# Kernel tuning notes

Hardware: AMD Instinct MI355X
Metric: run time of the kernel (lower is better)

Reference implementation:

```python
import jax, jax.numpy as jnp
import numpy as np

B, N = 16, 16384


def square_distance(a, b):
    # a [B,S,3], b [B,N,3] -> squared pairwise distance [B,S,N]
    return (jnp.sum(a * a, -1)[:, :, None]
            + jnp.sum(b * b, -1)[:, None, :]
            - 2.0 * jnp.einsum('bsc,bnc->bsn', a, b))


def fps(xyz, npoint):
    # farthest point sampling (deterministic start at index 0).
    b, n, _ = xyz.shape

    def step(carry, _):
        dist, far = carry
        cen = jnp.take_along_axis(xyz, far[:, None, None], axis=1)  # [B,1,3]
        d = jnp.sum((xyz - cen) ** 2, -1)
        dist = jnp.minimum(dist, d)
        return (dist, jnp.argmax(dist, -1)), far

    init = (jnp.full((b, n), 1e10, xyz.dtype), jnp.zeros((b,), jnp.int32))
    _, idx = jax.lax.scan(step, init, None, length=npoint)
    return idx.T  # [B, npoint]


def query_ball(radius, nsample, xyz, new_xyz):
    # torch query_ball_point: mark out-of-radius as N, sort, take first nsample,
    # replace leftover N with the first valid index.
    b, n, _ = xyz.shape
    sqr = square_distance(new_xyz, xyz)                      # [B,S,N]
    idx = jnp.broadcast_to(jnp.arange(n), sqr.shape)
    idx = jnp.where(sqr > radius * radius, n, idx)
    idx = jnp.sort(idx, axis=-1)[:, :, :nsample]             # [B,S,K]
    first = idx[:, :, :1]
    return jnp.where(idx == n, first, idx)


def index_points(points, idx):
    # points [B,N,C], idx [B,...] -> [B,...,C]
    return jax.vmap(lambda p, i: p[i])(points, idx)


def set_abstraction(xyz, points, npoint, radius, nsample, weights):
    new_xyz = index_points(xyz, fps(xyz, npoint))            # [B,S,3]
    idx = query_ball(radius, nsample, xyz, new_xyz)          # [B,S,K]
    grouped_xyz = index_points(xyz, idx) - new_xyz[:, :, None, :]  # [B,S,K,3]
    if points is None:
        feat = grouped_xyz
    else:
        feat = jnp.concatenate([grouped_xyz, index_points(points, idx)], axis=-1)
    for W, b_ in weights:                                    # 1x1 conv == per-point linear
        feat = jax.nn.relu(jnp.einsum('bskc,oc->bsko', feat, W) + b_)
    return new_xyz, jnp.max(feat, axis=2)                    # [B,S,Cout]


def setup_inputs() -> dict:
    key = jax.random.key(0)
    ks = jax.random.split(key, 13)
    xyz = jax.random.normal(ks[0], (B, N, 3), dtype=jnp.float32)

    def lin(k, cout, cin):
        return jax.random.normal(k, (cout, cin), dtype=jnp.float32) / np.sqrt(cin)

    return {
        'xyz': xyz,
        'sa1_w1': lin(ks[1], 64, 3),   'sa1_b1': jnp.zeros((64,), jnp.float32),
        'sa1_w2': lin(ks[2], 64, 64),  'sa1_b2': jnp.zeros((64,), jnp.float32),
        'sa1_w3': lin(ks[3], 128, 64), 'sa1_b3': jnp.zeros((128,), jnp.float32),
        'sa2_w1': lin(ks[4], 128, 131), 'sa2_b1': jnp.zeros((128,), jnp.float32),
        'sa2_w2': lin(ks[5], 256, 128), 'sa2_b2': jnp.zeros((256,), jnp.float32),
        'sa2_w3': lin(ks[6], 256, 256), 'sa2_b3': jnp.zeros((256,), jnp.float32),
    }


def reference(xyz, sa1_w1, sa1_b1, sa1_w2, sa1_b2, sa1_w3, sa1_b3,
              sa2_w1, sa2_b1, sa2_w2, sa2_b2, sa2_w3, sa2_b3):
    l1_xyz, l1_points = set_abstraction(
        xyz, None, 512, 0.04, 32,
        [(sa1_w1, sa1_b1), (sa1_w2, sa1_b2), (sa1_w3, sa1_b3)])
    l2_xyz, l2_points = set_abstraction(
        l1_xyz, l1_points, 128, 0.08, 64,
        [(sa2_w1, sa2_b1), (sa2_w2, sa2_b2), (sa2_w3, sa2_b3)])
    return l2_points  # [B, 128, 256] (channel-last == torch output after permute)
```

## Files before the change

### kernel.cpp

```cpp
#include <hip/hip_runtime.h>
#include <float.h>

#define NB 16
#define N1 16384
#define NP1 512
#define NS1 32
#define N2 512
#define NP2 128
#define NS2 64
#define TILE1 2048

__device__ __forceinline__ float sq3_np(float x, float y, float z) {
#pragma clang fp contract(off)
  return ((x * x) + (y * y)) + (z * z);
}
__device__ __forceinline__ float dot3_np(float ax, float ay, float az,
                                         float bx, float by, float bz) {
#pragma clang fp contract(off)
  return ((ax * bx) + (ay * by)) + (az * bz);
}
__device__ __forceinline__ float sqr_np(float ca, float sb, float dot) {
#pragma clang fp contract(off)
  return (ca + sb) - (2.0f * dot);
}
__device__ __forceinline__ float distmin_np(float px, float py, float pz,
                                            float cx, float cy, float cz,
                                            float old) {
#pragma clang fp contract(off)
  float dx = px - cx, dy = py - cy, dz = pz - cz;
  float d = ((dx * dx) + (dy * dy)) + (dz * dz);
  return d < old ? d : old;
}

constexpr size_t OFF_W1T1 = 0;
constexpr size_t OFF_W2T1 = 256;
constexpr size_t OFF_W3T1 = 4352;
constexpr size_t OFF_W1T2 = 12544;
constexpr size_t OFF_W2T2 = 29312;
constexpr size_t OFF_W3T2 = 62080;
constexpr size_t OFF_NORM1 = 127616;
constexpr size_t OFF_L1XYZ = 389760;
constexpr size_t OFF_NORM2 = 414336;
constexpr size_t OFF_L1PTS = 422528;
constexpr size_t OFF_FPS1I = 1471104;
constexpr size_t OFF_FPS2I = 1479296;
constexpr size_t WS_FLOATS = 1481344;

__global__ void prep_kernel(const float* __restrict__ xyz,
                            const float* __restrict__ w1a, const float* __restrict__ w2a,
                            const float* __restrict__ w3a, const float* __restrict__ w1b,
                            const float* __restrict__ w2b, const float* __restrict__ w3b,
                            float* __restrict__ ws) {
  int tid = blockIdx.x * blockDim.x + threadIdx.x;
  int stride = gridDim.x * blockDim.x;
  const int nNorm = NB * N1;
  const int e1 = nNorm + 192;
  const int e2 = e1 + 64 * 64;
  const int e3 = e2 + 128 * 64;
  const int e4 = e3 + 128 * 131;
  const int e5 = e4 + 256 * 128;
  const int e6 = e5 + 256 * 256;
  for (int i = tid; i < e6; i += stride) {
    if (i < nNorm) {
      ws[OFF_NORM1 + i] =
          sq3_np(xyz[(size_t)i * 3], xyz[(size_t)i * 3 + 1], xyz[(size_t)i * 3 + 2]);
    } else if (i < e1) {
      int j = i - nNorm; int o = j & 63, c = j >> 6;
      ws[OFF_W1T1 + j] = w1a[o * 3 + c];
    } else if (i < e2) {
      int j = i - e1; int o = j & 63, c = j >> 6;
      ws[OFF_W2T1 + j] = w2a[o * 64 + c];
    } else if (i < e3) {
      int j = i - e2; int o = j & 127, c = j >> 7;
      ws[OFF_W3T1 + j] = w3a[o * 64 + c];
    } else if (i < e4) {
      int j = i - e3; int o = j & 127, c = j >> 7;
      ws[OFF_W1T2 + j] = w1b[o * 131 + c];
    } else if (i < e5) {
      int j = i - e4; int o = j & 255, c = j >> 8;
      ws[OFF_W2T2 + j] = w2b[o * 128 + c];
    } else {
      int j = i - e5; int o = j & 255, c = j >> 8;
      ws[OFF_W3T2 + j] = w3b[o * 256 + c];
    }
  }
}

__global__ __launch_bounds__(512, 2) void fps1_kernel(const float* __restrict__ xyz,
                                                      int* __restrict__ out_idx) {
  int b = blockIdx.x;
  int t = threadIdx.x;
  int w = t >> 6, lane = t & 63;
  const float* xb = xyz + (size_t)b * N1 * 3;
  float px[32], py[32], pz[32], dist[32];
#pragma unroll
  for (int k = 0; k < 32; ++k) {
    int p = k * 512 + t;
    px[k] = xb[p * 3];
    py[k] = xb[p * 3 + 1];
    pz[k] = xb[p * 3 + 2];
    dist[k] = 1e10f;
  }
  __shared__ unsigned long long s_key[2][8];
  if (t == 0) out_idx[b * NP1] = 0;
  float cx = xb[0], cy = xb[1], cz = xb[2];
  for (int s = 1; s < NP1; ++s) {
    float bv = -1.0f; int bk = 0;
#pragma unroll
    for (int k = 0; k < 32; ++k) {
      float nd = distmin_np(px[k], py[k], pz[k], cx, cy, cz, dist[k]);
      dist[k] = nd;
      if (nd > bv) { bv = nd; bk = k; }
    }
    unsigned int gidx = ((unsigned int)bk << 9) | (unsigned int)t;
    unsigned long long key =
        ((unsigned long long)__float_as_uint(bv) << 32) | (unsigned int)~gidx;
#pragma unroll
    for (int off = 1; off < 64; off <<= 1) {
      unsigned long long ok = __shfl_xor(key, off);
      if (ok > key) key = ok;
    }
    if (lane == 0) s_key[s & 1][w] = key;
    __syncthreads();
    unsigned long long fk = s_key[s & 1][0];
#pragma unroll
    for (int i = 1; i < 8; ++i) {
      unsigned long long k2 = s_key[s & 1][i];
      if (k2 > fk) fk = k2;
    }
    unsigned int fi = ~(unsigned int)fk;
    cx = xb[fi * 3]; cy = xb[fi * 3 + 1]; cz = xb[fi * 3 + 2];
    if (t == 0) out_idx[b * NP1 + s] = (int)fi;
  }
}

__global__ __launch_bounds__(64) void fps2_kernel(const float* __restrict__ l1_xyz,
                                                  int* __restrict__ out_idx) {
  int b = blockIdx.x;
  int lane = threadIdx.x;
  const float* xb = l1_xyz + (size_t)b * N2 * 3;
  float px[8], py[8], pz[8], dist[8];
#pragma unroll
  for (int k = 0; k < 8; ++k) {
    int p = k * 64 + lane;
    px[k] = xb[p * 3]; py[k] = xb[p * 3 + 1]; pz[k] = xb[p * 3 + 2];
    dist[k] = 1e10f;
  }
  if (lane == 0) out_idx[b * NP2] = 0;
  float cx = xb[0], cy = xb[1], cz = xb[2];
  for (int s = 1; s < NP2; ++s) {
    float bv = -1.0f; int bi = 0;
    float wx = 0.f, wy = 0.f, wz = 0.f;
#pragma unroll
    for (int k = 0; k < 8; ++k) {
      float nd = distmin_np(px[k], py[k], pz[k], cx, cy, cz, dist[k]);
      dist[k] = nd;
      if (nd > bv) { bv = nd; bi = k * 64 + lane; wx = px[k]; wy = py[k]; wz = pz[k]; }
    }
#pragma unroll
    for (int off = 1; off < 64; off <<= 1) {
      float ov = __shfl_xor(bv, off);
      int oi = __shfl_xor(bi, off);
      float ox = __shfl_xor(wx, off), oy = __shfl_xor(wy, off), oz = __shfl_xor(wz, off);
      if (ov > bv || (ov == bv && oi < bi)) { bv = ov; bi = oi; wx = ox; wy = oy; wz = oz; }
    }
    cx = wx; cy = wy; cz = wz;
    if (lane == 0) out_idx[b * NP2 + s] = bi;
  }
}

__global__ __launch_bounds__(256) void sa1_kernel(
    const float* __restrict__ xyz, const float* __restrict__ norms1,
    const int* __restrict__ fps1_idx,
    const float* __restrict__ w1T, const float* __restrict__ bias1,
    const float* __restrict__ w2T, const float* __restrict__ bias2,
    const float* __restrict__ w3T, const float* __restrict__ bias3,
    float* __restrict__ l1_xyz, float* __restrict__ norms2, float* __restrict__ l1_pts) {
  __shared__ float4 tile[TILE1];
  __shared__ float blx[4 * NS1], bly[4 * NS1], blz[4 * NS1];
  int b = blockIdx.x >> 7;
  int t = threadIdx.x;
  int w = t >> 6, lane = t & 63;
  int s = ((blockIdx.x & 127) << 2) + w;
  const float* xb = xyz + (size_t)b * N1 * 3;
  const float* nb = norms1 + (size_t)b * N1;
  int cidx = fps1_idx[b * NP1 + s];
  float cx = xb[cidx * 3], cy = xb[cidx * 3 + 1], cz = xb[cidx * 3 + 2];
  float ca = nb[cidx];
  const float r2 = (float)(0.04 * 0.04);
  int tot = 0;
  for (int t0 = 0; t0 < N1; t0 += TILE1) {
    for (int i = t; i < TILE1; i += 256) {
      int p = t0 + i;
      tile[i] = make_float4(xb[p * 3], xb[p * 3 + 1], xb[p * 3 + 2], nb[p]);
    }
    __syncthreads();
    for (int j = 0; j < TILE1; j += 256) {
      float4 p0 = tile[j + lane];
      float4 p1 = tile[j + 64 + lane];
      float4 p2 = tile[j + 128 + lane];
      float4 p3 = tile[j + 192 + lane];
      bool in0 = !(sqr_np(ca, p0.w, dot3_np(cx, cy, cz, p0.x, p0.y, p0.z)) > r2);
      bool in1 = !(sqr_np(ca, p1.w, dot3_np(cx, cy, cz, p1.x, p1.y, p1.z)) > r2);
      bool in2 = !(sqr_np(ca, p2.w, dot3_np(cx, cy, cz, p2.x, p2.y, p2.z)) > r2);
      bool in3 = !(sqr_np(ca, p3.w, dot3_np(cx, cy, cz, p3.x, p3.y, p3.z)) > r2);
      unsigned long long any = __ballot(in0 | in1 | in2 | in3);
      if (any) {
#define SA1_APPEND(inq, pq)                                                     \
        {                                                                       \
          unsigned long long m = __ballot(inq);                                 \
          if (m) {                                                              \
            int rank = __popcll(m & ((1ull << lane) - 1ull));                   \
            int slot = tot + rank;                                              \
            if (inq && slot < NS1) {                                            \
              blx[w * NS1 + slot] = pq.x - cx;                                  \
              bly[w * NS1 + slot] = pq.y - cy;                                  \
              blz[w * NS1 + slot] = pq.z - cz;                                  \
            }                                                                   \
            tot += (int)__popcll(m);                                            \
            if (tot > NS1) tot = NS1;                                           \
          }                                                                     \
        }
        SA1_APPEND(in0, p0)
        SA1_APPEND(in1, p1)
        SA1_APPEND(in2, p2)
        SA1_APPEND(in3, p3)
#undef SA1_APPEND
      }
    }
    __syncthreads();
  }
  int cnt = tot > 0 ? tot : 1;
  float m0 = -FLT_MAX, m1 = -FLT_MAX;
  for (int k = 0; k < cnt; ++k) {
    float fx = blx[w * NS1 + k], fy = bly[w * NS1 + k], fz = blz[w * NS1 + k];
    float h1 = bias1[lane] + w1T[lane] * fx + w1T[64 + lane] * fy + w1T[128 + lane] * fz;
    h1 = fmaxf(h1, 0.0f);
    float a = bias2[lane];
#pragma unroll 8
    for (int c = 0; c < 64; ++c) a += w2T[c * 64 + lane] * __shfl(h1, c);
    a = fmaxf(a, 0.0f);
    float a0 = bias3[lane], a1 = bias3[64 + lane];
#pragma unroll 8
    for (int c = 0; c < 64; ++c) {
      float hv = __shfl(a, c);
      a0 += w3T[c * 128 + lane] * hv;
      a1 += w3T[c * 128 + 64 + lane] * hv;
    }
    a0 = fmaxf(a0, 0.0f); a1 = fmaxf(a1, 0.0f);
    m0 = fmaxf(m0, a0); m1 = fmaxf(m1, a1);
  }
  float* op = l1_pts + ((size_t)b * NP1 + s) * 128;
  op[lane] = m0;
  op[64 + lane] = m1;
  if (lane == 0) {
    float* xp = l1_xyz + ((size_t)b * NP1 + s) * 3;
    xp[0] = cx; xp[1] = cy; xp[2] = cz;
    norms2[b * NP1 + s] = ca;
  }
}

__global__ __launch_bounds__(256) void sa2_kernel(
    const float* __restrict__ l1_xyz, const float* __restrict__ norms2,
    const float* __restrict__ l1_pts, const int* __restrict__ fps2_idx,
    const float* __restrict__ w1T, const float* __restrict__ bias1,
    const float* __restrict__ w2T, const float* __restrict__ bias2,
    const float* __restrict__ w3T, const float* __restrict__ bias3,
    float* __restrict__ out) {
  __shared__ float sx[N2], sy[N2], sz[N2], sn[N2];
  __shared__ float blx[4 * NS2], bly[4 * NS2], blz[4 * NS2];
  __shared__ int bli[4 * NS2];
  int b = blockIdx.x >> 5;
  int t = threadIdx.x;
  int w = t >> 6, lane = t & 63;
  int s = ((blockIdx.x & 31) << 2) + w;
  const float* xb = l1_xyz + (size_t)b * N2 * 3;
  const float* nb = norms2 + (size_t)b * N2;
  for (int i = t; i < N2; i += 256) {
    sx[i] = xb[i * 3]; sy[i] = xb[i * 3 + 1]; sz[i] = xb[i * 3 + 2]; sn[i] = nb[i];
  }
  __syncthreads();
  int cidx = fps2_idx[b * NP2 + s];
  float cx = sx[cidx], cy = sy[cidx], cz = sz[cidx], ca = sn[cidx];
  const float r2 = (float)(0.08 * 0.08);
  int tot = 0;
  for (int j = 0; j < N2; j += 64) {
    int i = j + lane;
    float px = sx[i], py = sy[i], pz = sz[i], sb = sn[i];
    bool in = !(sqr_np(ca, sb, dot3_np(cx, cy, cz, px, py, pz)) > r2);
    unsigned long long m = __ballot(in);
    int rank = __popcll(m & ((1ull << lane) - 1ull));
    int slot = tot + rank;
    if (in && slot < NS2) {
      blx[w * NS2 + slot] = px - cx;
      bly[w * NS2 + slot] = py - cy;
      blz[w * NS2 + slot] = pz - cz;
      bli[w * NS2 + slot] = i;
    }
    tot += (int)__popcll(m);
    if (tot > NS2) tot = NS2;
  }
  __syncthreads();
  int cnt = tot > 0 ? tot : 1;
  float mx0 = -FLT_MAX, mx1 = -FLT_MAX, mx2 = -FLT_MAX, mx3 = -FLT_MAX;
  for (int k = 0; k < cnt; ++k) {
    float fx = blx[w * NS2 + k], fy = bly[w * NS2 + k], fz = blz[w * NS2 + k];
    int pidx = bli[w * NS2 + k];
    const float* fp = l1_pts + ((size_t)b * N2 + pidx) * 128;
    float a0 = bias1[lane] + w1T[lane] * fx + w1T[128 + lane] * fy + w1T[256 + lane] * fz;
    float a1 = bias1[64 + lane] + w1T[64 + lane] * fx + w1T[192 + lane] * fy + w1T[320 + lane] * fz;
#pragma unroll 4
    for (int c = 0; c < 128; ++c) {
      float fv = fp[c];
      a0 += w1T[(size_t)(3 + c) * 128 + lane] * fv;
      a1 += w1T[(size_t)(3 + c) * 128 + 64 + lane] * fv;
    }
    float h1a = fmaxf(a0, 0.0f), h1b = fmaxf(a1, 0.0f);
    float acc0 = bias2[lane], acc1 = bias2[64 + lane], acc2 = bias2[128 + lane], acc3 = bias2[192 + lane];
#pragma unroll 4
    for (int c = 0; c < 64; ++c) {
      float hv = __shfl(h1a, c);
      acc0 += w2T[(size_t)c * 256 + lane] * hv;
      acc1 += w2T[(size_t)c * 256 + 64 + lane] * hv;
      acc2 += w2T[(size_t)c * 256 + 128 + lane] * hv;
      acc3 += w2T[(size_t)c * 256 + 192 + lane] * hv;
    }
#pragma unroll 4
    for (int c = 0; c < 64; ++c) {
      float hv = __shfl(h1b, c);
      acc0 += w2T[(size_t)(64 + c) * 256 + lane] * hv;
      acc1 += w2T[(size_t)(64 + c) * 256 + 64 + lane] * hv;
      acc2 += w2T[(size_t)(64 + c) * 256 + 128 + lane] * hv;
      acc3 += w2T[(size_t)(64 + c) * 256 + 192 + lane] * hv;
    }
    float h20 = fmaxf(acc0, 0.0f), h21 = fmaxf(acc1, 0.0f);
    float h22 = fmaxf(acc2, 0.0f), h23 = fmaxf(acc3, 0.0f);
    float o0 = bias3[lane], o1 = bias3[64 + lane], o2 = bias3[128 + lane], o3 = bias3[192 + lane];
#define SA2_L3(hreg, rbase)                                                     \
    {                                                                           \
      _Pragma("unroll 4")                                                       \
      for (int c = 0; c < 64; ++c) {                                            \
        float hv = __shfl(hreg, c);                                             \
        o0 += w3T[(size_t)(rbase + c) * 256 + lane] * hv;                       \
        o1 += w3T[(size_t)(rbase + c) * 256 + 64 + lane] * hv;                  \
        o2 += w3T[(size_t)(rbase + c) * 256 + 128 + lane] * hv;                 \
        o3 += w3T[(size_t)(rbase + c) * 256 + 192 + lane] * hv;                 \
      }                                                                         \
    }
    SA2_L3(h20, 0)
    SA2_L3(h21, 64)
    SA2_L3(h22, 128)
    SA2_L3(h23, 192)
#undef SA2_L3
    mx0 = fmaxf(mx0, fmaxf(o0, 0.0f));
    mx1 = fmaxf(mx1, fmaxf(o1, 0.0f));
    mx2 = fmaxf(mx2, fmaxf(o2, 0.0f));
    mx3 = fmaxf(mx3, fmaxf(o3, 0.0f));
  }
  float* op = out + ((size_t)b * NP2 + s) * 256;
  op[lane] = mx0;
  op[64 + lane] = mx1;
  op[128 + lane] = mx2;
  op[192 + lane] = mx3;
}

extern "C" void kernel_launch(void* const* d_in, const int* in_sizes, int n_in,
                              void* d_out, int out_size, void* d_ws, size_t ws_size,
                              hipStream_t stream) {
  const float* xyz = (const float*)d_in[0];
  const float* sa1_w1 = (const float*)d_in[1];
  const float* sa1_b1 = (const float*)d_in[2];
  const float* sa1_w2 = (const float*)d_in[3];
  const float* sa1_b2 = (const float*)d_in[4];
  const float* sa1_w3 = (const float*)d_in[5];
  const float* sa1_b3 = (const float*)d_in[6];
  const float* sa2_w1 = (const float*)d_in[7];
  const float* sa2_b1 = (const float*)d_in[8];
  const float* sa2_w2 = (const float*)d_in[9];
  const float* sa2_b2 = (const float*)d_in[10];
  const float* sa2_w3 = (const float*)d_in[11];
  const float* sa2_b3 = (const float*)d_in[12];

  if (ws_size < WS_FLOATS * sizeof(float)) return;

  float* ws = (float*)d_ws;
  float* w1T1 = ws + OFF_W1T1;
  float* w2T1 = ws + OFF_W2T1;
  float* w3T1 = ws + OFF_W3T1;
  float* w1T2 = ws + OFF_W1T2;
  float* w2T2 = ws + OFF_W2T2;
  float* w3T2 = ws + OFF_W3T2;
  float* norms1 = ws + OFF_NORM1;
  float* l1xyz = ws + OFF_L1XYZ;
  float* norms2 = ws + OFF_NORM2;
  float* l1pts = ws + OFF_L1PTS;
  int* fps1i = (int*)(ws + OFF_FPS1I);
  int* fps2i = (int*)(ws + OFF_FPS2I);

  prep_kernel<<<1024, 256, 0, stream>>>(xyz, sa1_w1, sa1_w2, sa1_w3, sa2_w1, sa2_w2, sa2_w3, ws);
  fps1_kernel<<<NB, 512, 0, stream>>>(xyz, fps1i);
  sa1_kernel<<<NB * (NP1 / 4), 256, 0, stream>>>(xyz, norms1, fps1i, w1T1, sa1_b1, w2T1,
                                                 sa1_b2, w3T1, sa1_b3, l1xyz, norms2, l1pts);
  fps2_kernel<<<NB, 64, 0, stream>>>(l1xyz, fps2i);
  sa2_kernel<<<NB * (NP2 / 4), 256, 0, stream>>>(l1xyz, norms2, l1pts, fps2i, w1T2, sa2_b1,
                                                 w2T2, sa2_b2, w3T2, sa2_b3, (float*)d_out);
}
```

Measured before the change: 1.104 ms.

## Split FPS1 across eight cooperating blocks per batch with global mailbox sync

Farthest point sampling for level 1 is spread over 8 blocks per batch, each holding 2048 points, so 128 blocks run instead of 16. After each step the blocks exchange their local argmax key and coordinates through a zeroed global mailbox using release/acquire atomics and spin-waiting. The goal is to shorten the serial per-step distance update by using more CUs, at the cost of global-memory synchronization latency every step, and the scheme relies on all 128 blocks being co-resident to avoid deadlock. FPS2 now keeps its points in shared memory and reduces a packed 64-bit key instead of shuffling coordinates.

```diff
diff --git a/kernel.cpp b/kernel.cpp
--- a/kernel.cpp
+++ b/kernel.cpp
@@ -9,6 +9,7 @@
 #define NP2 128
 #define NS2 64
 #define TILE1 2048
+#define KS 8
 
 __device__ __forceinline__ float sq3_np(float x, float y, float z) {
 #pragma clang fp contract(off)
@@ -42,6 +43,7 @@
 constexpr size_t OFF_L1XYZ = 389760;
 constexpr size_t OFF_NORM2 = 414336;
 constexpr size_t OFF_L1PTS = 422528;
+constexpr size_t OFF_MBOX = OFF_L1PTS;
 constexpr size_t OFF_FPS1I = 1471104;
 constexpr size_t OFF_FPS2I = 1479296;
 constexpr size_t WS_FLOATS = 1481344;
@@ -87,85 +89,137 @@
 }
 
 __global__ __launch_bounds__(512, 2) void fps1_kernel(const float* __restrict__ xyz,
+                                                      unsigned long long* __restrict__ mb,
                                                       int* __restrict__ out_idx) {
-  int b = blockIdx.x;
-  int t = threadIdx.x;
-  int w = t >> 6, lane = t & 63;
-  const float* xb = xyz + (size_t)b * N1 * 3;
-  float px[32], py[32], pz[32], dist[32];
-#pragma unroll
-  for (int k = 0; k < 32; ++k) {
-    int p = k * 512 + t;
-    px[k] = xb[p * 3];
-    py[k] = xb[p * 3 + 1];
-    pz[k] = xb[p * 3 + 2];
-    dist[k] = 1e10f;
+  const int bid = blockIdx.x;
+  const int b = bid & 15, k = bid >> 4;
+  const int t = threadIdx.x, w = t >> 6, lane = t & 63;
+  const float* __restrict__ xb = xyz + (size_t)b * N1 * 3;
+  const int base = k * 2048;
+  float px[4], py[4], pz[4], dist[4];
+#pragma unroll
+  for (int j = 0; j < 4; ++j) {
+    int p = base + j * 512 + t;
+    px[j] = xb[3 * p]; py[j] = xb[3 * p + 1]; pz[j] = xb[3 * p + 2];
+    dist[j] = 1e10f;
   }
   __shared__ unsigned long long s_key[2][8];
-  if (t == 0) out_idx[b * NP1] = 0;
+  __shared__ float s_cx[2][8], s_cy[2][8], s_cz[2][8];
+  __shared__ unsigned long long s_gk[2];
+  __shared__ float s_gx[2], s_gy[2], s_gz[2];
+  if (k == 0 && t == 0) out_idx[b * NP1] = 0;
   float cx = xb[0], cy = xb[1], cz = xb[2];
   for (int s = 1; s < NP1; ++s) {
-    float bv = -1.0f; int bk = 0;
-#pragma unroll
-    for (int k = 0; k < 32; ++k) {
-      float nd = distmin_np(px[k], py[k], pz[k], cx, cy, cz, dist[k]);
+    const int par = s & 1;
+    unsigned long long bk = 0ull;
+    float bx = 0.f, by = 0.f, bz = 0.f;
+#pragma unroll
+    for (int j = 0; j < 4; ++j) {
+      float nd = distmin_np(px[j], py[j], pz[j], cx, cy, cz, dist[j]);
+      dist[j] = nd;
+      unsigned p = (unsigned)(base + j * 512 + t);
+      unsigned long long kk =
+          ((unsigned long long)__float_as_uint(nd) << 32) | (unsigned)~p;
+      if (kk > bk) { bk = kk; bx = px[j]; by = py[j]; bz = pz[j]; }
+    }
+#pragma unroll
+    for (int off = 1; off < 64; off <<= 1) {
+      unsigned long long ok = __shfl_xor(bk, off);
+      float ox = __shfl_xor(bx, off), oy = __shfl_xor(by, off), oz = __shfl_xor(bz, off);
+      if (ok > bk) { bk = ok; bx = ox; by = oy; bz = oz; }
+    }
+    if (lane == 0) {
+      s_key[par][w] = bk;
+      s_cx[par][w] = bx; s_cy[par][w] = by; s_cz[par][w] = bz;
+    }
+    __syncthreads();
+    if (w == 0) {
+      unsigned long long kk = (lane < 8) ? s_key[par][lane] : 0ull;
+      float xx = (lane < 8) ? s_cx[par][lane] : 0.f;
+      float yy = (lane < 8) ? s_cy[par][lane] : 0.f;
+      float zz = (lane < 8) ? s_cz[par][lane] : 0.f;
+#pragma unroll
+      for (int off = 1; off < 8; off <<= 1) {
+        unsigned long long ok = __shfl_xor(kk, off);
+        float ox = __shfl_xor(xx, off), oy = __shfl_xor(yy, off), oz = __shfl_xor(zz, off);
+        if (ok > kk) { kk = ok; xx = ox; yy = oy; zz = oz; }
+      }
+      if (lane == 0) {
+        unsigned long long* slot = mb + (((size_t)s * NB + b) * KS + k) * 4;
+        __hip_atomic_store(&slot[1], (unsigned long long)__float_as_uint(xx),
+                           __ATOMIC_RELAXED, __HIP_MEMORY_SCOPE_AGENT);
+        __hip_atomic_store(&slot[2], (unsigned long long)__float_as_uint(yy),
+                           __ATOMIC_RELAXED, __HIP_MEMORY_SCOPE_AGENT);
+        __hip_atomic_store(&slot[3], (unsigned long long)__float_as_uint(zz),
+                           __ATOMIC_RELAXED, __HIP_MEMORY_SCOPE_AGENT);
+        __hip_atomic_store(&slot[0], kk, __ATOMIC_RELEASE, __HIP_MEMORY_SCOPE_AGENT);
+      }
+      unsigned long long pk = 0ull;
+      float pxx = 0.f, pyy = 0.f, pzz = 0.f;
+      if (lane < 8) {
+        unsigned long long* ps = mb + (((size_t)s * NB + b) * KS + lane) * 4;
+        do {
+          pk = __hip_atomic_load(&ps[0], __ATOMIC_ACQUIRE, __HIP_MEMORY_SCOPE_AGENT);
+          if (!pk) __builtin_amdgcn_s_sleep(1);
+        } while (!pk);
+        pxx = __uint_as_float((unsigned)__hip_atomic_load(&ps[1], __ATOMIC_RELAXED,
+                                                          __HIP_MEMORY_SCOPE_AGENT));
+        pyy = __uint_as_float((unsigned)__hip_atomic_load(&ps[2], __ATOMIC_RELAXED,
+                                                          __HIP_MEMORY_SCOPE_AGENT));
+        pzz = __uint_as_float((unsigned)__hip_atomic_load(&ps[3], __ATOMIC_RELAXED,
+                                                          __HIP_MEMORY_SCOPE_AGENT));
+      }
+#pragma unroll
+      for (int off = 1; off < 8; off <<= 1) {
+        unsigned long long ok = __shfl_xor(pk, off);
+        float ox = __shfl_xor(pxx, off), oy = __shfl_xor(pyy, off), oz = __shfl_xor(pzz, off);
+        if (ok > pk) { pk = ok; pxx = ox; pyy = oy; pzz = oz; }
+      }
+      if (lane == 0) {
+        s_gk[par] = pk;
+        s_gx[par] = pxx; s_gy[par] = pyy; s_gz[par] = pzz;
+      }
+    }
+    __syncthreads();
+    cx = s_gx[par]; cy = s_gy[par]; cz = s_gz[par];
+    if (k == 0 && t == 0) out_idx[b * NP1 + s] = (int)~(unsigned)s_gk[par];
+  }
+}
+
+__global__ __launch_bounds__(64) void fps2_kernel(const float* __restrict__ l1_xyz,
+                                                  int* __restrict__ out_idx) {
+  __shared__ float spt[N2 * 3];
+  int b = blockIdx.x;
+  int lane = threadIdx.x;
+  const float* xb = l1_xyz + (size_t)b * N2 * 3;
+  for (int i = lane; i < N2 * 3; i += 64) spt[i] = xb[i];
+  float dist[8];
+#pragma unroll
+  for (int k = 0; k < 8; ++k) dist[k] = 1e10f;
+  if (lane == 0) out_idx[b * NP2] = 0;
+  float cx = xb[0], cy = xb[1], cz = xb[2];
+  __syncthreads();
+  for (int s = 1; s < NP2; ++s) {
+    float bv = -1.0f;
+    unsigned int gi = 0;
+#pragma unroll
+    for (int k = 0; k < 8; ++k) {
+      int p = k * 64 + lane;
+      float x = spt[3 * p], y = spt[3 * p + 1], z = spt[3 * p + 2];
+      float nd = distmin_np(x, y, z, cx, cy, cz, dist[k]);
       dist[k] = nd;
-      if (nd > bv) { bv = nd; bk = k; }
-    }
-    unsigned int gidx = ((unsigned int)bk << 9) | (unsigned int)t;
+      if (nd > bv) { bv = nd; gi = (unsigned)p; }
+    }
     unsigned long long key =
-        ((unsigned long long)__float_as_uint(bv) << 32) | (unsigned int)~gidx;
+        ((unsigned long long)__float_as_uint(bv) << 32) | (unsigned int)~gi;
 #pragma unroll
     for (int off = 1; off < 64; off <<= 1) {
       unsigned long long ok = __shfl_xor(key, off);
       if (ok > key) key = ok;
     }
-    if (lane == 0) s_key[s & 1][w] = key;
-    __syncthreads();
-    unsigned long long fk = s_key[s & 1][0];
-#pragma unroll
-    for (int i = 1; i < 8; ++i) {
-      unsigned long long k2 = s_key[s & 1][i];
-      if (k2 > fk) fk = k2;
-    }
-    unsigned int fi = ~(unsigned int)fk;
-    cx = xb[fi * 3]; cy = xb[fi * 3 + 1]; cz = xb[fi * 3 + 2];
-    if (t == 0) out_idx[b * NP1 + s] = (int)fi;
-  }
-}
-
-__global__ __launch_bounds__(64) void fps2_kernel(const float* __restrict__ l1_xyz,
-                                                  int* __restrict__ out_idx) {
-  int b = blockIdx.x;
-  int lane = threadIdx.x;
-  const float* xb = l1_xyz + (size_t)b * N2 * 3;
-  float px[8], py[8], pz[8], dist[8];
-#pragma unroll
-  for (int k = 0; k < 8; ++k) {
-    int p = k * 64 + lane;
-    px[k] = xb[p * 3]; py[k] = xb[p * 3 + 1]; pz[k] = xb[p * 3 + 2];
-    dist[k] = 1e10f;
-  }
-  if (lane == 0) out_idx[b * NP2] = 0;
-  float cx = xb[0], cy = xb[1], cz = xb[2];
-  for (int s = 1; s < NP2; ++s) {
-    float bv = -1.0f; int bi = 0;
-    float wx = 0.f, wy = 0.f, wz = 0.f;
-#pragma unroll
-    for (int k = 0; k < 8; ++k) {
-      float nd = distmin_np(px[k], py[k], pz[k], cx, cy, cz, dist[k]);
-      dist[k] = nd;
-      if (nd > bv) { bv = nd; bi = k * 64 + lane; wx = px[k]; wy = py[k]; wz = pz[k]; }
-    }
-#pragma unroll
-    for (int off = 1; off < 64; off <<= 1) {
-      float ov = __shfl_xor(bv, off);
-      int oi = __shfl_xor(bi, off);
-      float ox = __shfl_xor(wx, off), oy = __shfl_xor(wy, off), oz = __shfl_xor(wz, off);
-      if (ov > bv || (ov == bv && oi < bi)) { bv = ov; bi = oi; wx = ox; wy = oy; wz = oz; }
-    }
-    cx = wx; cy = wy; cz = wz;
-    if (lane == 0) out_idx[b * NP2 + s] = bi;
+    unsigned int fi = ~(unsigned int)key;
+    cx = spt[3 * fi]; cy = spt[3 * fi + 1]; cz = spt[3 * fi + 2];
+    if (lane == 0) out_idx[b * NP2 + s] = (int)fi;
   }
 }
 
@@ -394,11 +448,16 @@
   float* l1xyz = ws + OFF_L1XYZ;
   float* norms2 = ws + OFF_NORM2;
   float* l1pts = ws + OFF_L1PTS;
+  unsigned long long* mbox = (unsigned long long*)(ws + OFF_MBOX);
   int* fps1i = (int*)(ws + OFF_FPS1I);
   int* fps2i = (int*)(ws + OFF_FPS2I);
 
   prep_kernel<<<1024, 256, 0, stream>>>(xyz, sa1_w1, sa1_w2, sa1_w3, sa2_w1, sa2_w2, sa2_w3, ws);
-  fps1_kernel<<<NB, 512, 0, stream>>>(xyz, fps1i);
+
+  constexpr size_t MB_BYTES = (size_t)NP1 * NB * KS * 4 * sizeof(unsigned long long);
+  hipMemsetAsync(mbox, 0, MB_BYTES, stream);
+  fps1_kernel<<<NB * KS, 512, 0, stream>>>(xyz, mbox, fps1i);
+
   sa1_kernel<<<NB * (NP1 / 4), 256, 0, stream>>>(xyz, norms1, fps1i, w1T1, sa1_b1, w2T1,
                                                  sa1_b2, w3T1, sa1_b3, l1xyz, norms2, l1pts);
   fps2_kernel<<<NB, 64, 0, stream>>>(l1xyz, fps2i);
```

Result: slower. 2.373 ms (+114.9%).
